# Kernel optimization log

Measured on AMD Instinct MI355X. Metric: run time of the kernel, lower is better.

The kernel has to match this reference:

```python
import jax, jax.numpy as jnp
import numpy as np

IN_DIM = 256
OUT_DIM = 256
BS = 8
NODE = 256
BN_EPS = 1e-5


def setup_inputs() -> dict:
    key = jax.random.key(0)
    ks = jax.random.split(key, 9)
    s_in = 1.0 / np.sqrt(IN_DIM)
    return {
        "x": jax.random.normal(ks[0], (BS, NODE, IN_DIM), dtype=jnp.float32),
        # att_proj: Linear(in_dim, out_dim)
        "Wp": jax.random.uniform(ks[1], (IN_DIM, OUT_DIM), jnp.float32, -s_in, s_in),
        "bp": jax.random.uniform(ks[2], (OUT_DIM,), jnp.float32, -s_in, s_in),
        # att_weight: (out_dim, 1) xavier_normal -> keep as (out_dim,)
        "w_att": jax.random.normal(ks[3], (OUT_DIM,), jnp.float32) * np.sqrt(2.0 / (OUT_DIM + 1)),
        # proj_with_att: Linear(in_dim, out_dim)
        "W1": jax.random.uniform(ks[4], (IN_DIM, OUT_DIM), jnp.float32, -s_in, s_in),
        "b1": jax.random.uniform(ks[5], (OUT_DIM,), jnp.float32, -s_in, s_in),
        # proj_without_att: Linear(in_dim, out_dim)
        "W2": jax.random.uniform(ks[6], (IN_DIM, OUT_DIM), jnp.float32, -s_in, s_in),
        "b2": jax.random.uniform(ks[7], (OUT_DIM,), jnp.float32, -s_in, s_in),
        # BatchNorm1d affine params
        "gamma": jnp.ones((OUT_DIM,), jnp.float32),
        "beta": jnp.zeros((OUT_DIM,), jnp.float32),
    }


def reference(x, Wp, bp, w_att, W1, b1, W2, b2, gamma, beta):
    # dropout is identity in eval mode
    # pairwise mult + att_proj fused: (b,n,m,do) = (x_n * x_m) @ Wp + bp
    h = jnp.tanh(jnp.einsum('bnd,bmd,de->bnme', x, x, Wp) + bp)
    scores = jnp.einsum('bnme,e->bnm', h, w_att)          # (b, n, m)
    att = jax.nn.softmax(scores, axis=1)                  # softmax over dim=-2 of (b,n,m,1) => axis n
    agg = jnp.einsum('bnm,bmd->bnd', att, x)              # att_map.squeeze(-1) @ x
    out = (agg @ W1 + b1) + (x @ W2 + b2)                 # dual projection
    # BatchNorm1d over flattened (bs*node) batch axis (training-mode batch stats)
    flat = out.reshape(-1, out.shape[-1])
    mean = jnp.mean(flat, axis=0)
    var = jnp.var(flat, axis=0)
    out = (out - mean) * jax.lax.rsqrt(var + BN_EPS) * gamma + beta
    return jax.nn.selu(out)
```

## Files before the change

kernel.cpp:

```cpp
#include <hip/hip_runtime.h>
#include <hip/hip_bf16.h>
#include <stdint.h>

using f32x16 = __attribute__((ext_vector_type(16))) float;
using short8 = __attribute__((ext_vector_type(8))) short;

#define C2LOG2E 2.8853900817779268f

static __device__ __forceinline__ unsigned cvt_pk_bf16(float lo, float hi) {
  unsigned r;
  asm("v_cvt_pk_bf16_f32 %0, %1, %2" : "=v"(r) : "v"(lo), "v"(hi));
  return r;
}

template <int CTRL>
static __device__ __forceinline__ float dpp_add(float v) {
  int x = __builtin_amdgcn_update_dpp(0, __float_as_int(v), CTRL, 0xF, 0xF, true);
  return v + __int_as_float(x);
}
#define DPP_XOR1 0xB1
#define DPP_XOR2 0x4E
#define DPP_XOR4 0x141
#define DPP_XOR8 0x140

__device__ static const unsigned kMagicDiv[9] = {0u, 65536u, 32768u, 21846u, 16384u,
                                                 13108u, 10923u, 9363u, 8192u};

__global__ __launch_bounds__(256) void k_prep(const float* __restrict__ x,
                                              const float* __restrict__ Wp,
                                              unsigned int* __restrict__ xfrag,
                                              unsigned int* __restrict__ wpfrag) {
  const int bid = blockIdx.x, t = threadIdx.x;
  const int half = t >> 7, dpair = (t >> 5) & 3, rc = t & 31;
  const int kk = half * 8 + dpair * 2;
  if (bid < 1024) {
    const int b = bid >> 7, mt = (bid >> 4) & 7, ks = bid & 15;
    const int m = mt * 32 + rc;
    const int k = ks * 16 + kk;
    float2 v = *(const float2*)(x + (size_t)(b * 256 + m) * 256 + k);
    xfrag[(size_t)b * 32768 + ((mt * 16 + ks) << 8) + half * 128 + rc * 4 + dpair] =
        cvt_pk_bf16(v.x, v.y);
  } else {
    const int b2 = bid - 1024;
    const int et = b2 >> 4, ks = b2 & 15;
    const int e = et * 32 + rc;
    const int k = ks * 16 + kk;
    float v0 = Wp[(size_t)k * 256 + e];
    float v1 = Wp[(size_t)(k + 1) * 256 + e];
    wpfrag[((et * 16 + ks) << 8) + half * 128 + rc * 4 + dpair] = cvt_pk_bf16(v0, v1);
  }
}

__global__ __launch_bounds__(512, 4) void k_scores(
    const unsigned int* __restrict__ xfrag, const unsigned int* __restrict__ wpfrag,
    const float* __restrict__ bp, const float* __restrict__ watt,
    float* __restrict__ sp) {
  __shared__ unsigned char wplds[65536];

  const int tid = threadIdx.x;
  const int l = tid & 63, w = tid >> 6;
  const int c = l & 31, hi = l >> 5;
  const int h = blockIdx.x & 1;

  {
    const unsigned char* src = (const unsigned char*)wpfrag + (size_t)h * 65536;
    #pragma unroll
    for (int it = 0; it < 8; ++it) {
      __builtin_amdgcn_global_load_lds(
          (const __attribute__((address_space(1))) unsigned int*)(src + it * 8192 + w * 1024 + l * 16),
          (__attribute__((address_space(3))) unsigned int*)(&wplds[it * 8192 + w * 1024]),
          16, 0, 0);
    }
  }

  float bpe[4], wm2[4], Wl = 0.f;
  #pragma unroll
  for (int et = 0; et < 4; ++et) {
    float bv = bp[h * 128 + et * 32 + c];
    float wv = watt[h * 128 + et * 32 + c];
    bpe[et] = bv * C2LOG2E;
    wm2[et] = -2.f * wv;
    Wl += wv;
  }
  __syncthreads();

  const int gw = (blockIdx.x >> 1) * 8 + w;

  for (int i = gw; i < 9216; i += 2048) {
    int b = i / 1152;
    int r = i - b * 1152;
    int nt, cum;
    if      (r < 256)  { nt = 0; cum = 0; }
    else if (r < 480)  { nt = 1; cum = 256; }
    else if (r < 672)  { nt = 2; cum = 480; }
    else if (r < 832)  { nt = 3; cum = 672; }
    else if (r < 960)  { nt = 4; cum = 832; }
    else if (r < 1056) { nt = 5; cum = 960; }
    else               { nt = (r < 1120) ? 6 : 7; cum = (r < 1120) ? 1056 : 1120; }
    int rr = r - cum;
    int w8 = 8 - nt;
    int q0 = (int)(((unsigned)rr * kMagicDiv[w8]) >> 16);
    int n  = nt * 32 + q0;
    int mt = nt + (rr - q0 * w8);
    const int m0 = mt * 32;

    const unsigned char* xfb = (const unsigned char*)xfrag + (size_t)b * 131072;
    const unsigned char* xnbase = xfb + (nt << 14) + hi * 512 + q0 * 16;
    const unsigned char* xmbase = xfb + (mt << 14) + l * 16;

    f32x16 acc0, acc1, acc2, acc3;
    #pragma unroll
    for (int q = 0; q < 16; ++q) { acc0[q] = 0.f; acc1[q] = 0.f; acc2[q] = 0.f; acc3[q] = 0.f; }

    #pragma unroll 4
    for (int ks = 0; ks < 16; ++ks) {
      uint4 xnp = *(const uint4*)(xnbase + (ks << 10));
      uint4 xm  = *(const uint4*)(xmbase + (ks << 10));
      union U { uint4 u; short8 s; __hip_bfloat162 hh[4]; } a, mm, nn;
      mm.u = xm; nn.u = xnp;
      #pragma unroll
      for (int d = 0; d < 4; ++d) a.hh[d] = __hmul2(mm.hh[d], nn.hh[d]);

      short8 b0 = *(const short8*)(&wplds[((0 * 16 + ks) << 10) + l * 16]);
      short8 b1 = *(const short8*)(&wplds[((1 * 16 + ks) << 10) + l * 16]);
      short8 b2 = *(const short8*)(&wplds[((2 * 16 + ks) << 10) + l * 16]);
      short8 b3 = *(const short8*)(&wplds[((3 * 16 + ks) << 10) + l * 16]);
      acc0 = __builtin_amdgcn_mfma_f32_32x32x16_bf16(a.s, b0, acc0, 0, 0, 0);
      acc1 = __builtin_amdgcn_mfma_f32_32x32x16_bf16(a.s, b1, acc1, 0, 0, 0);
      acc2 = __builtin_amdgcn_mfma_f32_32x32x16_bf16(a.s, b2, acc2, 0, 0, 0);
      acc3 = __builtin_amdgcn_mfma_f32_32x32x16_bf16(a.s, b3, acc3, 0, 0, 0);
    }

    float p[16];
    #pragma unroll
    for (int q = 0; q < 16; ++q) {
      float v0 = fmaf(acc0[q], C2LOG2E, bpe[0]);
      float pq = fmaf(wm2[0], __builtin_amdgcn_rcpf(1.f + exp2f(v0)), Wl);
      float v1 = fmaf(acc1[q], C2LOG2E, bpe[1]);
      pq = fmaf(wm2[1], __builtin_amdgcn_rcpf(1.f + exp2f(v1)), pq);
      float v2 = fmaf(acc2[q], C2LOG2E, bpe[2]);
      pq = fmaf(wm2[2], __builtin_amdgcn_rcpf(1.f + exp2f(v2)), pq);
      float v3 = fmaf(acc3[q], C2LOG2E, bpe[3]);
      pq = fmaf(wm2[3], __builtin_amdgcn_rcpf(1.f + exp2f(v3)), pq);
      p[q] = pq;
    }

    #pragma unroll
    for (int q = 0; q < 16; ++q) {
      float v = p[q];
      v = dpp_add<DPP_XOR1>(v);
      v = dpp_add<DPP_XOR2>(v);
      v = dpp_add<DPP_XOR4>(v);
      v = dpp_add<DPP_XOR8>(v);
      v += __shfl_xor(v, 16);
      p[q] = v;
    }
    if (c == 0) {
      float* base = sp + (size_t)h * 524288;
      float* outrow = base + (size_t)(b * 256 + n) * 256 + m0;
      #pragma unroll
      for (int q = 0; q < 16; ++q) {
        int mr = (q & 3) + 8 * (q >> 2) + 4 * hi;
        outrow[mr] = p[q];
      }
      if (mt > nt) {
        #pragma unroll
        for (int q = 0; q < 16; ++q) {
          int mr = (q & 3) + 8 * (q >> 2) + 4 * hi;
          base[(size_t)(b * 256 + m0 + mr) * 256 + n] = p[q];
        }
      }
    }
  }
}

__global__ __launch_bounds__(256) void k_softmax(float* __restrict__ sp) {
  __shared__ float tile[256][65];
  __shared__ float red[4][64];
  const int t = threadIdx.x;
  const int bb = blockIdx.x >> 2, mt = blockIdx.x & 3;
  const int m0 = mt * 64;

  for (int c = 0; c < 64; ++c) {
    int nn = c * 4 + (t >> 6);
    size_t idx = (size_t)(bb * 256 + nn) * 256 + m0 + (t & 63);
    tile[nn][t & 63] = sp[idx] + sp[524288 + idx];
  }
  __syncthreads();
  const int col = t & 63, g = t >> 6;
  float mx = -1e30f;
  for (int k2 = 0; k2 < 64; ++k2) mx = fmaxf(mx, tile[g * 64 + k2][col]);
  red[g][col] = mx;
  __syncthreads();
  float M = fmaxf(fmaxf(red[0][col], red[1][col]), fmaxf(red[2][col], red[3][col]));
  float sm = 0.f;
  for (int k2 = 0; k2 < 64; ++k2) {
    float ev = __expf(tile[g * 64 + k2][col] - M);
    tile[g * 64 + k2][col] = ev;
    sm += ev;
  }
  __syncthreads();
  red[g][col] = sm;
  __syncthreads();
  float inv = 1.0f / (red[0][col] + red[1][col] + red[2][col] + red[3][col]);
  for (int k2 = 0; k2 < 64; ++k2) tile[g * 64 + k2][col] *= inv;
  __syncthreads();
  for (int c = 0; c < 64; ++c) {
    int nn = c * 4 + (t >> 6);
    sp[(size_t)(bb * 256 + nn) * 256 + m0 + (t & 63)] = tile[nn][t & 63];
  }
}

__global__ __launch_bounds__(256) void k_aggproj(
    const float* __restrict__ x, const float* __restrict__ att,
    const float* __restrict__ W1, const float* __restrict__ b1,
    const float* __restrict__ W2, const float* __restrict__ b2,
    float* __restrict__ out, float* __restrict__ bnpart) {
  __shared__ float att8[8][256];
  __shared__ float xn8[8][256];
  __shared__ float agg8[8][256];
  const int t = threadIdx.x;
  const int bb = blockIdx.x >> 5, ng = blockIdx.x & 31;
  const int n0 = ng * 8;

  #pragma unroll
  for (int i = 0; i < 8; ++i) {
    att8[i][t] = att[(size_t)(bb * 256 + n0 + i) * 256 + t];
    xn8[i][t]  = x  [(size_t)(bb * 256 + n0 + i) * 256 + t];
  }
  __syncthreads();

  float ar[8] = {0.f, 0.f, 0.f, 0.f, 0.f, 0.f, 0.f, 0.f};
  for (int m4 = 0; m4 < 64; ++m4) {
    int m = m4 * 4;
    float xv0 = x[(size_t)(bb * 256 + m + 0) * 256 + t];
    float xv1 = x[(size_t)(bb * 256 + m + 1) * 256 + t];
    float xv2 = x[(size_t)(bb * 256 + m + 2) * 256 + t];
    float xv3 = x[(size_t)(bb * 256 + m + 3) * 256 + t];
    #pragma unroll
    for (int i = 0; i < 8; ++i) {
      float4 av = *(const float4*)&att8[i][m];
      ar[i] += av.x * xv0 + av.y * xv1 + av.z * xv2 + av.w * xv3;
    }
  }
  #pragma unroll
  for (int i = 0; i < 8; ++i) agg8[i][t] = ar[i];
  __syncthreads();

  float o[8];
  float bsum = b1[t] + b2[t];
  #pragma unroll
  for (int i = 0; i < 8; ++i) o[i] = bsum;
  for (int d4 = 0; d4 < 64; ++d4) {
    int d = d4 * 4;
    float w10 = W1[(d + 0) * 256 + t], w11 = W1[(d + 1) * 256 + t];
    float w12 = W1[(d + 2) * 256 + t], w13 = W1[(d + 3) * 256 + t];
    float w20 = W2[(d + 0) * 256 + t], w21 = W2[(d + 1) * 256 + t];
    float w22 = W2[(d + 2) * 256 + t], w23 = W2[(d + 3) * 256 + t];
    #pragma unroll
    for (int i = 0; i < 8; ++i) {
      float4 ag = *(const float4*)&agg8[i][d];
      float4 xn = *(const float4*)&xn8[i][d];
      o[i] += ag.x * w10 + ag.y * w11 + ag.z * w12 + ag.w * w13
            + xn.x * w20 + xn.y * w21 + xn.z * w22 + xn.w * w23;
    }
  }
  float s1 = 0.f, s2 = 0.f;
  #pragma unroll
  for (int i = 0; i < 8; ++i) {
    out[(size_t)(bb * 256 + n0 + i) * 256 + t] = o[i];
    s1 += o[i];
    s2 += o[i] * o[i];
  }
  bnpart[(size_t)blockIdx.x * 512 + t]       = s1;
  bnpart[(size_t)blockIdx.x * 512 + 256 + t] = s2;
}

__global__ __launch_bounds__(256) void k_bnstats(const float* __restrict__ bnpart,
                                                 float* __restrict__ bnacc) {
  __shared__ float r4[4];
  const int s = blockIdx.x;
  const int t = threadIdx.x;
  float v = bnpart[(size_t)t * 512 + s];
  v += __shfl_xor(v, 1);
  v += __shfl_xor(v, 2);
  v += __shfl_xor(v, 4);
  v += __shfl_xor(v, 8);
  v += __shfl_xor(v, 16);
  v += __shfl_xor(v, 32);
  if ((t & 63) == 0) r4[t >> 6] = v;
  __syncthreads();
  if (t == 0) bnacc[s] = r4[0] + r4[1] + r4[2] + r4[3];
}

__global__ __launch_bounds__(256) void k_bnapply(float* __restrict__ io,
                                                 const float* __restrict__ bnacc,
                                                 const float* __restrict__ gamma,
                                                 const float* __restrict__ beta) {
  const int e = threadIdx.x;
  float mean = bnacc[e] * (1.0f / 2048.0f);
  float var  = bnacc[256 + e] * (1.0f / 2048.0f) - mean * mean;
  float scl  = rsqrtf(var + 1e-5f) * gamma[e];
  float sh   = beta[e] - mean * scl;
  for (int r = blockIdx.x; r < 2048; r += gridDim.x) {
    float v = io[(size_t)r * 256 + e];
    float y = v * scl + sh;
    float s = (y > 0.f) ? 1.0507009873554805f * y
                        : 1.7580993408473766f * (__expf(y) - 1.0f);
    io[(size_t)r * 256 + e] = s;
  }
}

extern "C" void kernel_launch(void* const* d_in, const int* in_sizes, int n_in,
                              void* d_out, int out_size, void* d_ws, size_t ws_size,
                              hipStream_t stream) {
  const float* x     = (const float*)d_in[0];
  const float* Wp    = (const float*)d_in[1];
  const float* bp    = (const float*)d_in[2];
  const float* watt  = (const float*)d_in[3];
  const float* W1    = (const float*)d_in[4];
  const float* b1    = (const float*)d_in[5];
  const float* W2    = (const float*)d_in[6];
  const float* b2    = (const float*)d_in[7];
  const float* gamma = (const float*)d_in[8];
  const float* beta  = (const float*)d_in[9];
  float* out = (float*)d_out;
  float* ws  = (float*)d_ws;

  float* sp = ws;
  unsigned int* wpfragG = (unsigned int*)(ws + 1048576);
  unsigned int* xfragG  = wpfragG + 32768;
  float* bnpart = ws + 524288;
  float* bnacc  = bnpart + 131072;

  k_prep   <<<1152, 256, 0, stream>>>(x, Wp, xfragG, wpfragG);
  k_scores <<<512,  512, 0, stream>>>(xfragG, wpfragG, bp, watt, sp);
  k_softmax<<<32,   256, 0, stream>>>(sp);
  k_aggproj<<<256,  256, 0, stream>>>(x, sp, W1, b1, W2, b2, out, bnpart);
  k_bnstats<<<512,  256, 0, stream>>>(bnpart, bnacc);
  k_bnapply<<<256,  256, 0, stream>>>(out, bnacc, gamma, beta);
}
```

Measured before the change: 128.7 us.

## Compute all 256 output features per wave in k_scores, dropping the half split

The score kernel previously split the 256 projection features across two blocks, each handling 128. Each wrote its own partial score plane, and the softmax summed the two planes. Now each wave handles all 8 feature tiles with 8 accumulators and a full 128KB of Wp in LDS. This halves the xn*xm product work and x fragment loads, and removes the second score plane and the extra read in softmax. The cost is higher register pressure (8 f32x16 accumulators), only one 128KB-LDS block per CU, and half as many blocks.

New measurement: 124.0 us. 1.04x faster.

```diff
diff --git a/kernel.cpp b/kernel.cpp
--- a/kernel.cpp
+++ b/kernel.cpp
@@ -51,21 +51,20 @@
   }
 }
 
-__global__ __launch_bounds__(512, 4) void k_scores(
+__global__ __launch_bounds__(512, 2) void k_scores(
     const unsigned int* __restrict__ xfrag, const unsigned int* __restrict__ wpfrag,
     const float* __restrict__ bp, const float* __restrict__ watt,
     float* __restrict__ sp) {
-  __shared__ unsigned char wplds[65536];
+  __shared__ unsigned char wplds[131072];
 
   const int tid = threadIdx.x;
   const int l = tid & 63, w = tid >> 6;
   const int c = l & 31, hi = l >> 5;
-  const int h = blockIdx.x & 1;
 
   {
-    const unsigned char* src = (const unsigned char*)wpfrag + (size_t)h * 65536;
-    #pragma unroll
-    for (int it = 0; it < 8; ++it) {
+    const unsigned char* src = (const unsigned char*)wpfrag;
+    #pragma unroll
+    for (int it = 0; it < 16; ++it) {
       __builtin_amdgcn_global_load_lds(
           (const __attribute__((address_space(1))) unsigned int*)(src + it * 8192 + w * 1024 + l * 16),
           (__attribute__((address_space(3))) unsigned int*)(&wplds[it * 8192 + w * 1024]),
@@ -73,18 +72,18 @@
     }
   }
 
-  float bpe[4], wm2[4], Wl = 0.f;
-  #pragma unroll
-  for (int et = 0; et < 4; ++et) {
-    float bv = bp[h * 128 + et * 32 + c];
-    float wv = watt[h * 128 + et * 32 + c];
+  float bpe[8], wm2[8], Wl = 0.f;
+  #pragma unroll
+  for (int et = 0; et < 8; ++et) {
+    float bv = bp[et * 32 + c];
+    float wv = watt[et * 32 + c];
     bpe[et] = bv * C2LOG2E;
     wm2[et] = -2.f * wv;
     Wl += wv;
   }
   __syncthreads();
 
-  const int gw = (blockIdx.x >> 1) * 8 + w;
+  const int gw = blockIdx.x * 8 + w;
 
   for (int i = gw; i < 9216; i += 2048) {
     int b = i / 1152;
@@ -108,11 +107,13 @@
     const unsigned char* xnbase = xfb + (nt << 14) + hi * 512 + q0 * 16;
     const unsigned char* xmbase = xfb + (mt << 14) + l * 16;
 
-    f32x16 acc0, acc1, acc2, acc3;
-    #pragma unroll
-    for (int q = 0; q < 16; ++q) { acc0[q] = 0.f; acc1[q] = 0.f; acc2[q] = 0.f; acc3[q] = 0.f; }
-
-    #pragma unroll 4
+    f32x16 acc[8];
+    #pragma unroll
+    for (int et = 0; et < 8; ++et)
+      #pragma unroll
+      for (int q = 0; q < 16; ++q) acc[et][q] = 0.f;
+
+    #pragma unroll 2
     for (int ks = 0; ks < 16; ++ks) {
       uint4 xnp = *(const uint4*)(xnbase + (ks << 10));
       uint4 xm  = *(const uint4*)(xmbase + (ks << 10));
@@ -121,27 +122,22 @@
       #pragma unroll
       for (int d = 0; d < 4; ++d) a.hh[d] = __hmul2(mm.hh[d], nn.hh[d]);
 
-      short8 b0 = *(const short8*)(&wplds[((0 * 16 + ks) << 10) + l * 16]);
-      short8 b1 = *(const short8*)(&wplds[((1 * 16 + ks) << 10) + l * 16]);
-      short8 b2 = *(const short8*)(&wplds[((2 * 16 + ks) << 10) + l * 16]);
-      short8 b3 = *(const short8*)(&wplds[((3 * 16 + ks) << 10) + l * 16]);
-      acc0 = __builtin_amdgcn_mfma_f32_32x32x16_bf16(a.s, b0, acc0, 0, 0, 0);
-      acc1 = __builtin_amdgcn_mfma_f32_32x32x16_bf16(a.s, b1, acc1, 0, 0, 0);
-      acc2 = __builtin_amdgcn_mfma_f32_32x32x16_bf16(a.s, b2, acc2, 0, 0, 0);
-      acc3 = __builtin_amdgcn_mfma_f32_32x32x16_bf16(a.s, b3, acc3, 0, 0, 0);
+      #pragma unroll
+      for (int et = 0; et < 8; ++et) {
+        short8 bf = *(const short8*)(&wplds[((et * 16 + ks) << 10) + l * 16]);
+        acc[et] = __builtin_amdgcn_mfma_f32_32x32x16_bf16(a.s, bf, acc[et], 0, 0, 0);
+      }
     }
 
     float p[16];
     #pragma unroll
     for (int q = 0; q < 16; ++q) {
-      float v0 = fmaf(acc0[q], C2LOG2E, bpe[0]);
-      float pq = fmaf(wm2[0], __builtin_amdgcn_rcpf(1.f + exp2f(v0)), Wl);
-      float v1 = fmaf(acc1[q], C2LOG2E, bpe[1]);
-      pq = fmaf(wm2[1], __builtin_amdgcn_rcpf(1.f + exp2f(v1)), pq);
-      float v2 = fmaf(acc2[q], C2LOG2E, bpe[2]);
-      pq = fmaf(wm2[2], __builtin_amdgcn_rcpf(1.f + exp2f(v2)), pq);
-      float v3 = fmaf(acc3[q], C2LOG2E, bpe[3]);
-      pq = fmaf(wm2[3], __builtin_amdgcn_rcpf(1.f + exp2f(v3)), pq);
+      float pq = Wl;
+      #pragma unroll
+      for (int et = 0; et < 8; ++et) {
+        float v = fmaf(acc[et][q], C2LOG2E, bpe[et]);
+        pq = fmaf(wm2[et], __builtin_amdgcn_rcpf(1.f + exp2f(v)), pq);
+      }
       p[q] = pq;
     }
 
@@ -156,8 +152,7 @@
       p[q] = v;
     }
     if (c == 0) {
-      float* base = sp + (size_t)h * 524288;
-      float* outrow = base + (size_t)(b * 256 + n) * 256 + m0;
+      float* outrow = sp + (size_t)(b * 256 + n) * 256 + m0;
       #pragma unroll
       for (int q = 0; q < 16; ++q) {
         int mr = (q & 3) + 8 * (q >> 2) + 4 * hi;
@@ -167,7 +162,7 @@
         #pragma unroll
         for (int q = 0; q < 16; ++q) {
           int mr = (q & 3) + 8 * (q >> 2) + 4 * hi;
-          base[(size_t)(b * 256 + m0 + mr) * 256 + n] = p[q];
+          sp[(size_t)(b * 256 + m0 + mr) * 256 + n] = p[q];
         }
       }
     }
@@ -183,8 +178,7 @@
 
   for (int c = 0; c < 64; ++c) {
     int nn = c * 4 + (t >> 6);
-    size_t idx = (size_t)(bb * 256 + nn) * 256 + m0 + (t & 63);
-    tile[nn][t & 63] = sp[idx] + sp[524288 + idx];
+    tile[nn][t & 63] = sp[(size_t)(bb * 256 + nn) * 256 + m0 + (t & 63)];
   }
   __syncthreads();
   const int col = t & 63, g = t >> 6;
@@ -328,13 +322,13 @@
   float* ws  = (float*)d_ws;
 
   float* sp = ws;
-  unsigned int* wpfragG = (unsigned int*)(ws + 1048576);
+  unsigned int* wpfragG = (unsigned int*)(ws + 524288);
   unsigned int* xfragG  = wpfragG + 32768;
-  float* bnpart = ws + 524288;
+  float* bnpart = (float*)(xfragG + 262144);
   float* bnacc  = bnpart + 131072;
 
   k_prep   <<<1152, 256, 0, stream>>>(x, Wp, xfragG, wpfragG);
-  k_scores <<<512,  512, 0, stream>>>(xfragG, wpfragG, bp, watt, sp);
+  k_scores <<<256,  512, 0, stream>>>(xfragG, wpfragG, bp, watt, sp);
   k_softmax<<<32,   256, 0, stream>>>(sp);
   k_aggproj<<<256,  256, 0, stream>>>(x, sp, W1, b1, W2, b2, out, bnpart);
   k_bnstats<<<512,  256, 0, stream>>>(bnpart, bnacc);
```
